# Performance work log

Hardware: AMD Instinct MI355X
Metric: run time of the kernel (lower is better)

## Reference

```python
import jax, jax.numpy as jnp
import numpy as np

H, D = 16, 64          # num_heads, head_dim
OUT = H * D            # out_dim = 1024
W1, W2 = 32, 32        # sliding windows
EPS_NORM = 1e-7
EPS_LN = 1e-5


def setup_inputs() -> dict:
    key = jax.random.key(0)
    ks = jax.random.split(key, 6)
    B, S, IN = 2, 2048, 1024
    x = jax.random.normal(ks[0], (B, S, IN), dtype=jnp.float32)
    scale = 0.02
    W_Q = jax.random.normal(ks[1], (IN, OUT), dtype=jnp.float32) * scale
    W_K = jax.random.normal(ks[2], (IN, OUT), dtype=jnp.float32) * scale
    W_V = jax.random.normal(ks[3], (IN, OUT), dtype=jnp.float32) * scale
    W_Kp = jax.random.normal(ks[4], (IN, OUT), dtype=jnp.float32) * scale
    W_O = jax.random.normal(ks[5], (OUT, OUT), dtype=jnp.float32) * scale
    ln_gamma = jnp.ones((OUT,), dtype=jnp.float32)
    ln_beta = jnp.zeros((OUT,), dtype=jnp.float32)
    return {"x": x, "W_Q": W_Q, "W_K": W_K, "W_V": W_V, "W_Kp": W_Kp,
            "W_O": W_O, "ln_gamma": ln_gamma, "ln_beta": ln_beta}


def _l2norm(t):
    return t / (jnp.linalg.norm(t, axis=-1, keepdims=True) + EPS_NORM)


def reference(x, W_Q, W_K, W_V, W_Kp, W_O, ln_gamma, ln_beta):
    B, S, _ = x.shape
    # projections -> (B, S, H, D)
    Q = _l2norm((x @ W_Q).reshape(B, S, H, D))
    K = _l2norm((x @ W_K).reshape(B, S, H, D))
    Kp = _l2norm((x @ W_Kp).reshape(B, S, H, D))
    V = (x @ W_V).reshape(B, S, H, D)
    # windowed keys/values (last w1/w2 positions, as in the PyTorch fallback)
    K_win = K[:, -W1:]
    Kp_win = Kp[:, -W2:]
    V_win = V[:, -W1:]
    Vp_win = V[:, -W2:]
    # triple product A_ijk = q.k.k' / sqrt(D) -> (B, S, H, w1, w2)
    A = jnp.einsum('bshd,bjhd,bkhd->bshjk', Q, K_win, Kp_win) / jnp.sqrt(jnp.float32(D))
    # causal window mask: allow j <= i + w1 - S and k <= i + w2 - S
    s_idx = jnp.arange(S)[:, None, None]
    j_idx = jnp.arange(W1)[None, :, None]
    k_idx = jnp.arange(W2)[None, None, :]
    mask = (j_idx > s_idx + (W1 - S)) | (k_idx > s_idx + (W2 - S))  # (S, w1, w2)
    neg_inf = jnp.float32(-jnp.inf)
    A = jnp.where(mask[None, :, None, :, :], neg_inf, A)
    # joint softmax over (j, k); fully-masked query rows produce zeros
    A_flat = A.reshape(B, S, H, W1 * W2)
    all_masked = jnp.all(A_flat == neg_inf, axis=-1, keepdims=True)
    A_safe = jnp.where(all_masked, 0.0, A_flat)
    P = jax.nn.softmax(A_safe, axis=-1)
    P = jnp.where(all_masked, 0.0, P).reshape(B, S, H, W1, W2)
    # value outer-product weighting (V' = V)
    Z = jnp.einsum('bshjk,bjhd,bkhd->bshd', P, V_win, Vp_win)
    out = Z.reshape(B, S, OUT) @ W_O
    out = out + x  # residual (shapes match)
    # LayerNorm
    mu = jnp.mean(out, axis=-1, keepdims=True)
    var = jnp.mean((out - mu) ** 2, axis=-1, keepdims=True)
    out = (out - mu) / jnp.sqrt(var + EPS_LN) * ln_gamma + ln_beta
    return out
```

## Files before the change

kernel.cpp:

```cpp
#include <hip/hip_runtime.h>
#include <math.h>


#define XS 68
#define WS 68
#define PS 36

#define YP_STR   262144
#define NKS_P    8
#define YN_OFF   (NKS_P * YP_STR)
#define DP_OFF   (YN_OFF + 262144)
#define DP_STR   65536

__device__ __forceinline__ void ln_row(
    const float4* __restrict__ x4, const float4* __restrict__ g4,
    const float4* __restrict__ b4, float4* __restrict__ out4,
    int row, int lane) {
  float4 v[4];
  #pragma unroll
  for (int i = 0; i < 4; i++) v[i] = x4[row * 256 + i * 64 + lane];
  float sum = 0.f, ss = 0.f;
  #pragma unroll
  for (int i = 0; i < 4; i++) {
    sum += v[i].x + v[i].y + v[i].z + v[i].w;
    ss  += v[i].x * v[i].x + v[i].y * v[i].y + v[i].z * v[i].z + v[i].w * v[i].w;
  }
  #pragma unroll
  for (int off = 1; off < 64; off <<= 1) {
    sum += __shfl_xor(sum, off);
    ss  += __shfl_xor(ss, off);
  }
  float mu   = sum * (1.f / 1024.f);
  float rstd = rsqrtf(ss * (1.f / 1024.f) - mu * mu + 1e-5f);
  #pragma unroll
  for (int i = 0; i < 4; i++) {
    float4 g  = g4[i * 64 + lane];
    float4 be = b4[i * 64 + lane];
    float4 o;
    o.x = (v[i].x - mu) * rstd * g.x + be.x;
    o.y = (v[i].y - mu) * rstd * g.y + be.y;
    o.z = (v[i].z - mu) * rstd * g.z + be.z;
    o.w = (v[i].w - mu) * rstd * g.w + be.w;
    out4[row * 256 + i * 64 + lane] = o;
  }
}

__global__ __launch_bounds__(256, 4) void proj_ln_kernel(
    const float* __restrict__ x,
    const float* __restrict__ Wq, const float* __restrict__ Wk,
    const float* __restrict__ Wkp, const float* __restrict__ Wv,
    const float* __restrict__ gam, const float* __restrict__ bet,
    float* __restrict__ Y, float* __restrict__ out) {
  __shared__ float xs[64 * WS];
  __shared__ float wl[64 * WS];
  const int tid = threadIdx.x;
  const int bid = blockIdx.x;

  if (bid < 512) {
    const int cb   = bid & 63;
    const int ks   = bid >> 6;
    const int col0 = cb * 64;
    const int z    = cb >> 4;
    const int colz = col0 & 1023;
    const float* __restrict__ W =
        (z == 0) ? Wq : ((z == 1) ? Wk : ((z == 2) ? Wkp : Wv));
    const int tc = tid & 15, tr = tid >> 4;

    float acc[4][4];
    #pragma unroll
    for (int i = 0; i < 4; i++)
      #pragma unroll
      for (int j = 0; j < 4; j++) acc[i][j] = 0.f;

    for (int cc = 0; cc < 2; cc++) {
      const int kb = ks * 128 + cc * 64;
      #pragma unroll
      for (int i = 0; i < 4; i++) {
        int e = i * 256 + tid;
        int r = e >> 4, q = e & 15;
        int b = r >> 5, t = r & 31;
        float4 v = *(const float4*)(x + ((b * 2048 + 2016 + t) * 1024 + kb + q * 4));
        xs[(q * 4 + 0) * WS + r] = v.x;
        xs[(q * 4 + 1) * WS + r] = v.y;
        xs[(q * 4 + 2) * WS + r] = v.z;
        xs[(q * 4 + 3) * WS + r] = v.w;
        float4 w = *(const float4*)(W + (size_t)(kb + r) * 1024 + colz + q * 4);
        *(float4*)(wl + r * WS + q * 4) = w;
      }
      __syncthreads();

      #pragma unroll 8
      for (int kk = 0; kk < 64; kk++) {
        float4 xv = *(const float4*)(xs + kk * WS + tr * 4);
        float4 wv = *(const float4*)(wl + kk * WS + tc * 4);
        acc[0][0] = fmaf(xv.x, wv.x, acc[0][0]);
        acc[0][1] = fmaf(xv.x, wv.y, acc[0][1]);
        acc[0][2] = fmaf(xv.x, wv.z, acc[0][2]);
        acc[0][3] = fmaf(xv.x, wv.w, acc[0][3]);
        acc[1][0] = fmaf(xv.y, wv.x, acc[1][0]);
        acc[1][1] = fmaf(xv.y, wv.y, acc[1][1]);
        acc[1][2] = fmaf(xv.y, wv.z, acc[1][2]);
        acc[1][3] = fmaf(xv.y, wv.w, acc[1][3]);
        acc[2][0] = fmaf(xv.z, wv.x, acc[2][0]);
        acc[2][1] = fmaf(xv.z, wv.y, acc[2][1]);
        acc[2][2] = fmaf(xv.z, wv.z, acc[2][2]);
        acc[2][3] = fmaf(xv.z, wv.w, acc[2][3]);
        acc[3][0] = fmaf(xv.w, wv.x, acc[3][0]);
        acc[3][1] = fmaf(xv.w, wv.y, acc[3][1]);
        acc[3][2] = fmaf(xv.w, wv.z, acc[3][2]);
        acc[3][3] = fmaf(xv.w, wv.w, acc[3][3]);
      }
      __syncthreads();
    }

    float* __restrict__ Yo = Y + ks * YP_STR + col0;
    #pragma unroll
    for (int i = 0; i < 4; i++) {
      float4 o = make_float4(acc[i][0], acc[i][1], acc[i][2], acc[i][3]);
      *(float4*)(Yo + (tr * 4 + i) * 4096 + tc * 4) = o;
    }
  } else {
    const int wave = tid >> 6, lane = tid & 63;
    const int gw = (bid - 512) * 4 + wave;
    const float4* x4 = (const float4*)x;
    const float4* g4 = (const float4*)gam;
    const float4* b4 = (const float4*)bet;
    float4* out4 = (float4*)out;
    for (int idx = gw; idx < 4032; idx += 1792) {
      int row = (idx < 2016) ? idx : idx + 32;
      ln_row(x4, g4, b4, out4, row, lane);
    }
  }
}

__global__ __launch_bounds__(256, 8) void reduce_norm_kernel(
    const float* __restrict__ Yp, float* __restrict__ Yn) {
  const int tid  = threadIdx.x;
  const int wave = tid >> 6, lane = tid & 63;
  const int task = blockIdx.x * 4 + wave;
  const int r    = task & 63;
  const int h    = (task >> 6) & 15;
  const int arr  = task >> 10;
  const int off  = r * 4096 + arr * 1024 + h * 64 + lane;

  float v = 0.f;
  #pragma unroll
  for (int p = 0; p < NKS_P; p++) v += Yp[p * YP_STR + off];

  if (arr < 3) {
    float s2 = v * v;
    #pragma unroll
    for (int o = 1; o < 64; o <<= 1) s2 += __shfl_xor(s2, o);
    v *= (1.f / (sqrtf(s2) + 1e-7f));
  }
  Yn[off] = v;
}

__global__ __launch_bounds__(256, 1) void attn_wo_kernel(
    const float* __restrict__ Yn, const float* __restrict__ Wo,
    float* __restrict__ Dp) {
  __shared__ float Kn[32 * XS], Kp[32 * XS], Vs[32 * XS];
  __shared__ float Pt[4][32 * PS];
  __shared__ float qs[4][64];
  __shared__ float Zs[4][64];
  const int tid = threadIdx.x;
  const int wave = tid >> 6, lane = tid & 63;
  const int bid = blockIdx.x;
  const int h = bid & 15, b = (bid >> 4) & 1, mb = bid >> 5;

  #pragma unroll
  for (int i = 0; i < 6; i++) {
    int e = i * 256 + tid;
    int a = e >> 9;
    int rem = e & 511;
    int row = rem >> 4, q = rem & 15;
    float4 v = *(const float4*)(Yn + (b * 32 + row) * 4096 + (a + 1) * 1024 + h * 64 + q * 4);
    float* dst = (a == 0) ? Kn : ((a == 1) ? Kp : Vs);
    *(float4*)(dst + row * XS + q * 4) = v;
  }
  __syncthreads();

  const int m = mb * 4 + wave;
  const int r = b * 32 + m;

  float q = Yn[r * 4096 + h * 64 + lane];
  qs[wave][lane] = q;
  __builtin_amdgcn_wave_barrier();

  const int lj = lane >> 3, lk = lane & 7;
  float acc[4][4];
  #pragma unroll
  for (int a = 0; a < 4; a++)
    #pragma unroll
    for (int c = 0; c < 4; c++) acc[a][c] = 0.f;

  const float* qw = qs[wave];
  for (int dq = 0; dq < 16; dq++) {
    float4 q4 = *(const float4*)(qw + dq * 4);
    float4 t4[4], kp4[4];
    #pragma unroll
    for (int tj = 0; tj < 4; tj++) {
      float4 kv = *(const float4*)(Kn + (lj * 4 + tj) * XS + dq * 4);
      t4[tj].x = q4.x * kv.x; t4[tj].y = q4.y * kv.y;
      t4[tj].z = q4.z * kv.z; t4[tj].w = q4.w * kv.w;
    }
    #pragma unroll
    for (int tk = 0; tk < 4; tk++)
      kp4[tk] = *(const float4*)(Kp + (lk * 4 + tk) * XS + dq * 4);
    #pragma unroll
    for (int tj = 0; tj < 4; tj++)
      #pragma unroll
      for (int tk = 0; tk < 4; tk++)
        acc[tj][tk] += t4[tj].x * kp4[tk].x + t4[tj].y * kp4[tk].y
                     + t4[tj].z * kp4[tk].z + t4[tj].w * kp4[tk].w;
  }

  float amax = -1e30f;
  #pragma unroll
  for (int tj = 0; tj < 4; tj++)
    #pragma unroll
    for (int tk = 0; tk < 4; tk++) {
      int j = lj * 4 + tj, k = lk * 4 + tk;
      if (j <= m && k <= m) amax = fmaxf(amax, acc[tj][tk] * 0.125f);
    }
  #pragma unroll
  for (int off = 1; off < 64; off <<= 1) amax = fmaxf(amax, __shfl_xor(amax, off));

  float lsum = 0.f;
  float* ptw = Pt[wave];
  #pragma unroll
  for (int tj = 0; tj < 4; tj++)
    #pragma unroll
    for (int tk = 0; tk < 4; tk++) {
      int j = lj * 4 + tj, k = lk * 4 + tk;
      float e = 0.f;
      if (j <= m && k <= m) e = __expf(acc[tj][tk] * 0.125f - amax);
      lsum += e;
      ptw[k * PS + j] = e;
    }
  #pragma unroll
  for (int off = 1; off < 64; off <<= 1) lsum += __shfl_xor(lsum, off);
  float inv = 1.f / lsum;
  __builtin_amdgcn_wave_barrier();

  float vreg[32];
  #pragma unroll
  for (int k = 0; k < 32; k++) vreg[k] = Vs[k * XS + lane];

  float zacc = 0.f;
  #pragma unroll
  for (int k = 0; k < 32; k++) {
    float g = 0.f;
    #pragma unroll
    for (int j4 = 0; j4 < 8; j4++) {
      float4 p4 = *(const float4*)(ptw + k * PS + j4 * 4);
      g += p4.x * vreg[j4 * 4 + 0] + p4.y * vreg[j4 * 4 + 1]
         + p4.z * vreg[j4 * 4 + 2] + p4.w * vreg[j4 * 4 + 3];
    }
    zacc = fmaf(g, vreg[k], zacc);
  }
  Zs[wave][lane] = zacc * inv;
  __syncthreads();

  float wacc[4][4];
  #pragma unroll
  for (int i = 0; i < 4; i++)
    #pragma unroll
    for (int j = 0; j < 4; j++) wacc[i][j] = 0.f;

  const float* __restrict__ WoS = Wo + (size_t)h * 65536 + tid * 4;
  #pragma unroll 4
  for (int k = 0; k < 64; k++) {
    float4 wv = *(const float4*)(WoS + (size_t)k * 1024);
    #pragma unroll
    for (int rr = 0; rr < 4; rr++) {
      float zz = Zs[rr][k];
      wacc[rr][0] = fmaf(zz, wv.x, wacc[rr][0]);
      wacc[rr][1] = fmaf(zz, wv.y, wacc[rr][1]);
      wacc[rr][2] = fmaf(zz, wv.z, wacc[rr][2]);
      wacc[rr][3] = fmaf(zz, wv.w, wacc[rr][3]);
    }
  }
  const int r0 = b * 32 + mb * 4;
  float* __restrict__ D = Dp + h * DP_STR;
  #pragma unroll
  for (int rr = 0; rr < 4; rr++) {
    float4 o = make_float4(wacc[rr][0], wacc[rr][1], wacc[rr][2], wacc[rr][3]);
    *(float4*)(D + (size_t)(r0 + rr) * 1024 + tid * 4) = o;
  }
}

__global__ __launch_bounds__(256, 4) void ln_win_kernel(
    const float4* __restrict__ x4, const float4* __restrict__ dp4,
    const float4* __restrict__ g4, const float4* __restrict__ b4,
    float4* __restrict__ out4) {
  const int tid = threadIdx.x;
  const int wave = tid >> 6, lane = tid & 63;
  const int wr  = blockIdx.x * 4 + wave;
  const int row = (wr >> 5) * 2048 + 2016 + (wr & 31);

  float4 v[4];
  #pragma unroll
  for (int i = 0; i < 4; i++) v[i] = x4[row * 256 + i * 64 + lane];
  #pragma unroll
  for (int p = 0; p < 16; p++) {
    #pragma unroll
    for (int i = 0; i < 4; i++) {
      float4 d = dp4[p * 16384 + wr * 256 + i * 64 + lane];
      v[i].x += d.x; v[i].y += d.y; v[i].z += d.z; v[i].w += d.w;
    }
  }
  float sum = 0.f, ss = 0.f;
  #pragma unroll
  for (int i = 0; i < 4; i++) {
    sum += v[i].x + v[i].y + v[i].z + v[i].w;
    ss  += v[i].x * v[i].x + v[i].y * v[i].y + v[i].z * v[i].z + v[i].w * v[i].w;
  }
  #pragma unroll
  for (int off = 1; off < 64; off <<= 1) {
    sum += __shfl_xor(sum, off);
    ss  += __shfl_xor(ss, off);
  }
  float mu   = sum * (1.f / 1024.f);
  float rstd = rsqrtf(ss * (1.f / 1024.f) - mu * mu + 1e-5f);

  #pragma unroll
  for (int i = 0; i < 4; i++) {
    float4 g = g4[i * 64 + lane];
    float4 be = b4[i * 64 + lane];
    float4 o;
    o.x = (v[i].x - mu) * rstd * g.x + be.x;
    o.y = (v[i].y - mu) * rstd * g.y + be.y;
    o.z = (v[i].z - mu) * rstd * g.z + be.z;
    o.w = (v[i].w - mu) * rstd * g.w + be.w;
    out4[row * 256 + i * 64 + lane] = o;
  }
}

extern "C" void kernel_launch(void* const* d_in, const int* in_sizes, int n_in,
                              void* d_out, int out_size, void* d_ws, size_t ws_size,
                              hipStream_t stream) {
  const float* x   = (const float*)d_in[0];
  const float* Wq  = (const float*)d_in[1];
  const float* Wk  = (const float*)d_in[2];
  const float* Wv  = (const float*)d_in[3];
  const float* Wkp = (const float*)d_in[4];
  const float* Wo  = (const float*)d_in[5];
  const float* gam = (const float*)d_in[6];
  const float* bet = (const float*)d_in[7];
  float* out = (float*)d_out;
  float* ws  = (float*)d_ws;

  hipLaunchKernelGGL(proj_ln_kernel, dim3(512 + 448), dim3(256), 0, stream,
                     x, Wq, Wk, Wkp, Wv, gam, bet, ws, out);
  hipLaunchKernelGGL(reduce_norm_kernel, dim3(1024), dim3(256), 0, stream,
                     ws, ws + YN_OFF);
  hipLaunchKernelGGL(attn_wo_kernel, dim3(256), dim3(256), 0, stream,
                     ws + YN_OFF, Wo, ws + DP_OFF);
  hipLaunchKernelGGL(ln_win_kernel, dim3(16), dim3(256), 0, stream,
                     (const float4*)x, (const float4*)(ws + DP_OFF),
                     (const float4*)gam, (const float4*)bet, (float4*)out);
}
```

Measured before the change: 124.4 us.

## Fuse split-K reduction and L2 norm into attention kernel, drop reduce kernel

```diff
diff --git a/kernel.cpp b/kernel.cpp
--- a/kernel.cpp
+++ b/kernel.cpp
@@ -7,9 +7,8 @@
 #define PS 36
 
 #define YP_STR   262144
-#define NKS_P    8
-#define YN_OFF   (NKS_P * YP_STR)
-#define DP_OFF   (YN_OFF + 262144)
+#define NKS_P    4
+#define DP_OFF   (NKS_P * YP_STR)
 #define DP_STR   65536
 
 __device__ __forceinline__ void ln_row(
@@ -56,7 +55,7 @@
   const int tid = threadIdx.x;
   const int bid = blockIdx.x;
 
-  if (bid < 512) {
+  if (bid < 256) {
     const int cb   = bid & 63;
     const int ks   = bid >> 6;
     const int col0 = cb * 64;
@@ -72,8 +71,8 @@
       #pragma unroll
       for (int j = 0; j < 4; j++) acc[i][j] = 0.f;
 
-    for (int cc = 0; cc < 2; cc++) {
-      const int kb = ks * 128 + cc * 64;
+    for (int cc = 0; cc < 4; cc++) {
+      const int kb = ks * 256 + cc * 64;
       #pragma unroll
       for (int i = 0; i < 4; i++) {
         int e = i * 256 + tid;
@@ -121,7 +120,7 @@
     }
   } else {
     const int wave = tid >> 6, lane = tid & 63;
-    const int gw = (bid - 512) * 4 + wave;
+    const int gw = (bid - 256) * 4 + wave;
     const float4* x4 = (const float4*)x;
     const float4* g4 = (const float4*)gam;
     const float4* b4 = (const float4*)bet;
@@ -133,31 +132,8 @@
   }
 }
 
-__global__ __launch_bounds__(256, 8) void reduce_norm_kernel(
-    const float* __restrict__ Yp, float* __restrict__ Yn) {
-  const int tid  = threadIdx.x;
-  const int wave = tid >> 6, lane = tid & 63;
-  const int task = blockIdx.x * 4 + wave;
-  const int r    = task & 63;
-  const int h    = (task >> 6) & 15;
-  const int arr  = task >> 10;
-  const int off  = r * 4096 + arr * 1024 + h * 64 + lane;
-
-  float v = 0.f;
-  #pragma unroll
-  for (int p = 0; p < NKS_P; p++) v += Yp[p * YP_STR + off];
-
-  if (arr < 3) {
-    float s2 = v * v;
-    #pragma unroll
-    for (int o = 1; o < 64; o <<= 1) s2 += __shfl_xor(s2, o);
-    v *= (1.f / (sqrtf(s2) + 1e-7f));
-  }
-  Yn[off] = v;
-}
-
 __global__ __launch_bounds__(256, 1) void attn_wo_kernel(
-    const float* __restrict__ Yn, const float* __restrict__ Wo,
+    const float* __restrict__ Yp, const float* __restrict__ Wo,
     float* __restrict__ Dp) {
   __shared__ float Kn[32 * XS], Kp[32 * XS], Vs[32 * XS];
   __shared__ float Pt[4][32 * PS];
@@ -174,16 +150,44 @@
     int a = e >> 9;
     int rem = e & 511;
     int row = rem >> 4, q = rem & 15;
-    float4 v = *(const float4*)(Yn + (b * 32 + row) * 4096 + (a + 1) * 1024 + h * 64 + q * 4);
+    const float* src = Yp + (b * 32 + row) * 4096 + (a + 1) * 1024 + h * 64 + q * 4;
+    float4 acc4 = make_float4(0.f, 0.f, 0.f, 0.f);
+    #pragma unroll
+    for (int p = 0; p < NKS_P; p++) {
+      float4 v = *(const float4*)(src + p * YP_STR);
+      acc4.x += v.x; acc4.y += v.y; acc4.z += v.z; acc4.w += v.w;
+    }
     float* dst = (a == 0) ? Kn : ((a == 1) ? Kp : Vs);
-    *(float4*)(dst + row * XS + q * 4) = v;
+    *(float4*)(dst + row * XS + q * 4) = acc4;
+  }
+  __syncthreads();
+
+  for (int rr = 0; rr < 8; rr++) {
+    int row = wave * 8 + rr;
+    float kv = Kn[row * XS + lane];
+    float s2 = kv * kv;
+    #pragma unroll
+    for (int off = 1; off < 64; off <<= 1) s2 += __shfl_xor(s2, off);
+    Kn[row * XS + lane] = kv * (1.f / (sqrtf(s2) + 1e-7f));
+    float pv = Kp[row * XS + lane];
+    float p2 = pv * pv;
+    #pragma unroll
+    for (int off = 1; off < 64; off <<= 1) p2 += __shfl_xor(p2, off);
+    Kp[row * XS + lane] = pv * (1.f / (sqrtf(p2) + 1e-7f));
   }
   __syncthreads();
 
   const int m = mb * 4 + wave;
   const int r = b * 32 + m;
 
-  float q = Yn[r * 4096 + h * 64 + lane];
+  float q = 0.f;
+  #pragma unroll
+  for (int p = 0; p < NKS_P; p++)
+    q += Yp[p * YP_STR + r * 4096 + h * 64 + lane];
+  float q2 = q * q;
+  #pragma unroll
+  for (int off = 1; off < 64; off <<= 1) q2 += __shfl_xor(q2, off);
+  q *= (1.f / (sqrtf(q2) + 1e-7f));
   qs[wave][lane] = q;
   __builtin_amdgcn_wave_barrier();
 
@@ -294,47 +298,40 @@
     const float4* __restrict__ x4, const float4* __restrict__ dp4,
     const float4* __restrict__ g4, const float4* __restrict__ b4,
     float4* __restrict__ out4) {
+  __shared__ float red[8];
   const int tid = threadIdx.x;
   const int wave = tid >> 6, lane = tid & 63;
-  const int wr  = blockIdx.x * 4 + wave;
+  const int wr  = blockIdx.x;
   const int row = (wr >> 5) * 2048 + 2016 + (wr & 31);
 
-  float4 v[4];
-  #pragma unroll
-  for (int i = 0; i < 4; i++) v[i] = x4[row * 256 + i * 64 + lane];
+  float4 v = x4[row * 256 + tid];
   #pragma unroll
   for (int p = 0; p < 16; p++) {
-    #pragma unroll
-    for (int i = 0; i < 4; i++) {
-      float4 d = dp4[p * 16384 + wr * 256 + i * 64 + lane];
-      v[i].x += d.x; v[i].y += d.y; v[i].z += d.z; v[i].w += d.w;
-    }
-  }
-  float sum = 0.f, ss = 0.f;
-  #pragma unroll
-  for (int i = 0; i < 4; i++) {
-    sum += v[i].x + v[i].y + v[i].z + v[i].w;
-    ss  += v[i].x * v[i].x + v[i].y * v[i].y + v[i].z * v[i].z + v[i].w * v[i].w;
-  }
+    float4 d = dp4[p * 16384 + wr * 256 + tid];
+    v.x += d.x; v.y += d.y; v.z += d.z; v.w += d.w;
+  }
+  float s  = v.x + v.y + v.z + v.w;
+  float ss = v.x * v.x + v.y * v.y + v.z * v.z + v.w * v.w;
   #pragma unroll
   for (int off = 1; off < 64; off <<= 1) {
-    sum += __shfl_xor(sum, off);
-    ss  += __shfl_xor(ss, off);
-  }
+    s  += __shfl_xor(s, off);
+    ss += __shfl_xor(ss, off);
+  }
+  if (lane == 0) { red[wave] = s; red[4 + wave] = ss; }
+  __syncthreads();
+  float sum = red[0] + red[1] + red[2] + red[3];
+  float sq  = red[4] + red[5] + red[6] + red[7];
   float mu   = sum * (1.f / 1024.f);
-  float rstd = rsqrtf(ss * (1.f / 1024.f) - mu * mu + 1e-5f);
-
-  #pragma unroll
-  for (int i = 0; i < 4; i++) {
-    float4 g = g4[i * 64 + lane];
-    float4 be = b4[i * 64 + lane];
-    float4 o;
-    o.x = (v[i].x - mu) * rstd * g.x + be.x;
-    o.y = (v[i].y - mu) * rstd * g.y + be.y;
-    o.z = (v[i].z - mu) * rstd * g.z + be.z;
-    o.w = (v[i].w - mu) * rstd * g.w + be.w;
-    out4[row * 256 + i * 64 + lane] = o;
-  }
+  float rstd = rsqrtf(sq * (1.f / 1024.f) - mu * mu + 1e-5f);
+
+  float4 g  = g4[tid];
+  float4 be = b4[tid];
+  float4 o;
+  o.x = (v.x - mu) * rstd * g.x + be.x;
+  o.y = (v.y - mu) * rstd * g.y + be.y;
+  o.z = (v.z - mu) * rstd * g.z + be.z;
+  o.w = (v.w - mu) * rstd * g.w + be.w;
+  out4[row * 256 + tid] = o;
 }
 
 extern "C" void kernel_launch(void* const* d_in, const int* in_sizes, int n_in,
@@ -351,13 +348,11 @@
   float* out = (float*)d_out;
   float* ws  = (float*)d_ws;
 
-  hipLaunchKernelGGL(proj_ln_kernel, dim3(512 + 448), dim3(256), 0, stream,
+  hipLaunchKernelGGL(proj_ln_kernel, dim3(256 + 448), dim3(256), 0, stream,
                      x, Wq, Wk, Wkp, Wv, gam, bet, ws, out);
-  hipLaunchKernelGGL(reduce_norm_kernel, dim3(1024), dim3(256), 0, stream,
-                     ws, ws + YN_OFF);
   hipLaunchKernelGGL(attn_wo_kernel, dim3(256), dim3(256), 0, stream,
-                     ws + YN_OFF, Wo, ws + DP_OFF);
-  hipLaunchKernelGGL(ln_win_kernel, dim3(16), dim3(256), 0, stream,
+                     ws, Wo, ws + DP_OFF);
+  hipLaunchKernelGGL(ln_win_kernel, dim3(64), dim3(256), 0, stream,
                      (const float4*)x, (const float4*)(ws + DP_OFF),
                      (const float4*)gam, (const float4*)bet, (float4*)out);
 }
```

Result: no change. 125.1 us (+0.6%).
